# Kernel tuning notes

Measured on AMD Instinct MI355X. Metric: run time of the kernel, lower is better.

## Reference

```python
import jax, jax.numpy as jnp
import numpy as np

N = 50000      # nodes
E = 800000     # edges (avg degree 16)
F_IN = 128     # input feature dim
HID = 128      # 2 * out_classes
OUT = 64       # out_classes


def setup_inputs() -> dict:
    key = jax.random.key(0)
    ks = jax.random.split(key, 12)
    x = jax.random.normal(ks[0], (N, F_IN), jnp.float32)
    edge_index = jax.random.randint(ks[1], (2, E), 0, N, jnp.int32)
    def lin(k, fi, fo):
        return jax.random.normal(k, (fi, fo), jnp.float32) / np.float32(np.sqrt(fi))
    return {
        "x": x,
        "edge_index": edge_index,
        "W1": lin(ks[2], F_IN, HID), "b1": jnp.zeros((HID,), jnp.float32),
        "W2": lin(ks[3], HID, HID),  "b2": jnp.zeros((HID,), jnp.float32),
        "W3": lin(ks[4], HID, HID),  "b3": jnp.zeros((HID,), jnp.float32),
        "jk_w": jax.random.normal(ks[5], (3,), jnp.float32),
        "fc_W": lin(ks[6], HID, OUT), "fc_b": jnp.zeros((OUT,), jnp.float32),
    }


def _gcn_conv(h, W, b, row, col, n):
    """PyG GCNConv: linear -> add self-loops -> sym-normalized aggregate -> bias."""
    h = h @ W                                        # [n, d_out]
    loops = jnp.arange(n, dtype=row.dtype)
    r = jnp.concatenate([row, loops])                # sources
    c = jnp.concatenate([col, loops])                # targets
    deg = jax.ops.segment_sum(jnp.ones_like(c, h.dtype), c, num_segments=n)
    dinv = jnp.where(deg > 0, jax.lax.rsqrt(deg), 0.0)
    norm = dinv[r] * dinv[c]                         # [E+n]
    msg = h[r] * norm[:, None]                       # gather + scale
    return jax.ops.segment_sum(msg, c, num_segments=n) + b


def _neighbor_mean(h, row, col, n):
    """sample_neighbors with scale_factor=2: exact mean over out-neighbors,
    own feature when degree == 0 (top-k branch is provably dead code)."""
    s = jax.ops.segment_sum(h[col], row, num_segments=n)
    deg = jax.ops.segment_sum(jnp.ones_like(row, h.dtype), row, num_segments=n)
    mean = s / jnp.maximum(deg, 1.0)[:, None]
    return jnp.where((deg > 0)[:, None], mean, h)


def reference(x, edge_index, W1, b1, W2, b2, W3, b3, jk_w, fc_W, fc_b):
    row, col = edge_index[0], edge_index[1]
    n = x.shape[0]
    # layer 0: GCN -> ReLU -> (dropout: eval identity) -> neighbor sampling
    h0 = jax.nn.relu(_gcn_conv(x, W1, b1, row, col, n))
    h0 = _neighbor_mean(h0, row, col, n)
    # layer 1: GCN -> ReLU; historical-activation update is identity on first call
    h1 = jax.nn.relu(_gcn_conv(h0, W2, b2, row, col, n))
    # layer 2
    h2 = jax.nn.relu(_gcn_conv(h1, W3, b3, row, col, n))
    # dynamic JK aggregation
    w = jax.nn.softmax(jk_w)
    h = w[0] * h0 + w[1] * h1 + w[2] * h2
    return h @ fc_W + fc_b
```

## Files before the change

kernel.cpp:

```cpp
#include <hip/hip_runtime.h>
#include <stdint.h>

typedef unsigned int  uint32;
typedef unsigned short u16;

typedef short bfx8 __attribute__((ext_vector_type(8)));
typedef float f32x4 __attribute__((ext_vector_type(4)));
typedef float f32x2 __attribute__((ext_vector_type(2)));

#define NBP 256
#define CH  2048

__device__ __forceinline__ float b2f(u16 u) {
    union { uint32 i; float f; } v; v.i = ((uint32)u) << 16; return v.f;
}
__device__ __forceinline__ u16 f2b(float f) {
    union { float f; uint32 i; } v; v.f = f;
    uint32 u = v.i;
    return (u16)((u + 0x7fffu + ((u >> 16) & 1u)) >> 16);
}
__device__ __forceinline__ float blo(uint32 u) {
    union { uint32 i; float f; } v; v.i = u << 16; return v.f;
}
__device__ __forceinline__ float bhi(uint32 u) {
    union { uint32 i; float f; } v; v.i = u & 0xffff0000u; return v.f;
}
__device__ __forceinline__ uint32 packbf(float a, float b) {
    return (uint32)f2b(a) | ((uint32)f2b(b) << 16);
}
__device__ __forceinline__ void splitf(float x, u16& h, u16& l) {
    h = f2b(x);
    l = f2b(x - b2f(h));
}
__device__ __forceinline__ void split8(const float* __restrict__ p, bfx8& hi, bfx8& lo) {
    f32x4 a = *(const f32x4*)p;
    f32x4 b = *(const f32x4*)(p + 4);
    float x[8] = {a[0], a[1], a[2], a[3], b[0], b[1], b[2], b[3]};
#pragma unroll
    for (int j = 0; j < 8; ++j) {
        u16 h, l; splitf(x[j], h, l);
        hi[j] = (short)h; lo[j] = (short)l;
    }
}

__global__ __launch_bounds__(256) void k_preA(
    const int* __restrict__ row, const int* __restrict__ col, int E, int Gh,
    int* __restrict__ cntC, int* __restrict__ cntR, int* __restrict__ deg_in,
    const float* __restrict__ W1, const float* __restrict__ W2,
    const float* __restrict__ W3, const float* __restrict__ fcW,
    u16* __restrict__ WTh, u16* __restrict__ WTl, int WTN) {
    if ((int)blockIdx.x < Gh) {
        __shared__ int hp[NBP];
        int t = threadIdx.x;
        hp[t] = 0;
        __syncthreads();
        int base = blockIdx.x * CH;
        int n = E - base; if (n > CH) n = CH;
        for (int i = t; i < n; i += 256) {
            int r = row[base + i], c = col[base + i];
            atomicAdd(&hp[c >> 8], 1);
            atomicAdd(&hp[r >> 8], 0x10000);
            atomicAdd(&deg_in[c], 1);
        }
        __syncthreads();
        int v = hp[t];
        if (v & 0xffff) atomicAdd(&cntC[t], v & 0xffff);
        if (v >> 16)    atomicAdd(&cntR[t], v >> 16);
        return;
    }
    int i = ((int)blockIdx.x - Gh) * 256 + threadIdx.x;
    if (i >= WTN) return;
    float w;
    if (i < 3 * 16384) {
        int m = i >> 14, j = i & 16383;
        int fo = j >> 7, fi = j & 127;
        const float* W = (m == 0) ? W1 : (m == 1) ? W2 : W3;
        w = W[fi * 128 + fo];
    } else {
        int j = i - 3 * 16384;
        int fo = j >> 7, fi = j & 127;
        w = fcW[fi * 64 + fo];
    }
    u16 h, l; splitf(w, h, l);
    WTh[i] = h; WTl[i] = l;
}

__global__ __launch_bounds__(256) void k_scanB(
    const int* __restrict__ cntC, const int* __restrict__ cntR,
    int* __restrict__ bOffC, int* __restrict__ bOffR,
    int* __restrict__ curC, int* __restrict__ curR,
    const int* __restrict__ deg_in, float* __restrict__ dinv, int NB, int N) {
    int t = threadIdx.x;
    if (blockIdx.x >= 1) {
        int i = ((int)blockIdx.x - 1) * 256 + t;
        if (i < N) dinv[i] = rsqrtf((float)(deg_in[i] + 1));
        return;
    }
    int lane = t & 63, wid = t >> 6;
    __shared__ int wsum[4];
    for (int m = 0; m < 2; ++m) {
        const int* cnt = m ? cntR : cntC;
        int* bOff = m ? bOffR : bOffC;
        int* cur  = m ? curR  : curC;
        int v = (t < NB) ? cnt[t] : 0;
        int x = v;
#pragma unroll
        for (int d = 1; d < 64; d <<= 1) {
            int u = __shfl_up(x, d);
            if (lane >= d) x += u;
        }
        if (lane == 63) wsum[wid] = x;
        __syncthreads();
        int add = 0;
        for (int i = 0; i < wid; ++i) add += wsum[i];
        int ex = x + add - v;
        if (t <= NB) bOff[t] = ex;
        cur[t] = ex;
        __syncthreads();
    }
}

__device__ __forceinline__ void gemm128_f32_body(
    const float* __restrict__ A, const u16* __restrict__ WTh, const u16* __restrict__ WTl,
    const float* __restrict__ dinv, u16* __restrict__ G, int M, int blk) {
    const int lane = threadIdx.x & 63;
    const int q = lane >> 4, l = lane & 15;
    int rbase = blk * 128 + (threadIdx.x >> 6) * 32;
    if (rbase >= M) return;
    int r0 = rbase + l;      if (r0 >= M) r0 = M - 1;
    int r1 = rbase + 16 + l; if (r1 >= M) r1 = M - 1;

    f32x4 acc[2][8];
#pragma unroll
    for (int i = 0; i < 2; ++i)
#pragma unroll
        for (int j = 0; j < 8; ++j) acc[i][j] = (f32x4){0.f, 0.f, 0.f, 0.f};

#pragma unroll
    for (int kc = 0; kc < 4; ++kc) {
        int k0 = kc * 32 + q * 8;
        bfx8 ah0, al0, ah1, al1;
        split8(A + (size_t)r0 * 128 + k0, ah0, al0);
        split8(A + (size_t)r1 * 128 + k0, ah1, al1);
#pragma unroll
        for (int ct = 0; ct < 8; ++ct) {
            bfx8 bh = *(const bfx8*)(WTh + (ct * 16 + l) * 128 + k0);
            bfx8 bl = *(const bfx8*)(WTl + (ct * 16 + l) * 128 + k0);
            acc[0][ct] = __builtin_amdgcn_mfma_f32_16x16x32_bf16(ah0, bh, acc[0][ct], 0, 0, 0);
            acc[0][ct] = __builtin_amdgcn_mfma_f32_16x16x32_bf16(ah0, bl, acc[0][ct], 0, 0, 0);
            acc[0][ct] = __builtin_amdgcn_mfma_f32_16x16x32_bf16(al0, bh, acc[0][ct], 0, 0, 0);
            acc[1][ct] = __builtin_amdgcn_mfma_f32_16x16x32_bf16(ah1, bh, acc[1][ct], 0, 0, 0);
            acc[1][ct] = __builtin_amdgcn_mfma_f32_16x16x32_bf16(ah1, bl, acc[1][ct], 0, 0, 0);
            acc[1][ct] = __builtin_amdgcn_mfma_f32_16x16x32_bf16(al1, bh, acc[1][ct], 0, 0, 0);
        }
    }
#pragma unroll
    for (int rs = 0; rs < 2; ++rs) {
#pragma unroll
        for (int rr = 0; rr < 4; ++rr) {
            int rw = rbase + rs * 16 + q * 4 + rr;
            if (rw < M) {
                float dv = dinv[rw];
#pragma unroll
                for (int ct = 0; ct < 8; ++ct)
                    G[(size_t)rw * 128 + ct * 16 + l] = f2b(acc[rs][ct][rr] * dv);
            }
        }
    }
}

__global__ __launch_bounds__(256) void k_gemm128_pl(
    const u16* __restrict__ Ah, const u16* __restrict__ Al,
    const u16* __restrict__ WTh, const u16* __restrict__ WTl,
    const float* __restrict__ dinv, u16* __restrict__ G, int M) {
    const int lane = threadIdx.x & 63;
    const int q = lane >> 4, l = lane & 15;
    int rbase = blockIdx.x * 128 + (threadIdx.x >> 6) * 32;
    if (rbase >= M) return;
    int r0 = rbase + l;      if (r0 >= M) r0 = M - 1;
    int r1 = rbase + 16 + l; if (r1 >= M) r1 = M - 1;

    f32x4 acc[2][8];
#pragma unroll
    for (int i = 0; i < 2; ++i)
#pragma unroll
        for (int j = 0; j < 8; ++j) acc[i][j] = (f32x4){0.f, 0.f, 0.f, 0.f};

#pragma unroll
    for (int kc = 0; kc < 4; ++kc) {
        int k0 = kc * 32 + q * 8;
        bfx8 ah0 = *(const bfx8*)(Ah + (size_t)r0 * 128 + k0);
        bfx8 al0 = *(const bfx8*)(Al + (size_t)r0 * 128 + k0);
        bfx8 ah1 = *(const bfx8*)(Ah + (size_t)r1 * 128 + k0);
        bfx8 al1 = *(const bfx8*)(Al + (size_t)r1 * 128 + k0);
#pragma unroll
        for (int ct = 0; ct < 8; ++ct) {
            bfx8 bh = *(const bfx8*)(WTh + (ct * 16 + l) * 128 + k0);
            bfx8 bl = *(const bfx8*)(WTl + (ct * 16 + l) * 128 + k0);
            acc[0][ct] = __builtin_amdgcn_mfma_f32_16x16x32_bf16(ah0, bh, acc[0][ct], 0, 0, 0);
            acc[0][ct] = __builtin_amdgcn_mfma_f32_16x16x32_bf16(ah0, bl, acc[0][ct], 0, 0, 0);
            acc[0][ct] = __builtin_amdgcn_mfma_f32_16x16x32_bf16(al0, bh, acc[0][ct], 0, 0, 0);
            acc[1][ct] = __builtin_amdgcn_mfma_f32_16x16x32_bf16(ah1, bh, acc[1][ct], 0, 0, 0);
            acc[1][ct] = __builtin_amdgcn_mfma_f32_16x16x32_bf16(ah1, bl, acc[1][ct], 0, 0, 0);
            acc[1][ct] = __builtin_amdgcn_mfma_f32_16x16x32_bf16(al1, bh, acc[1][ct], 0, 0, 0);
        }
    }
#pragma unroll
    for (int rs = 0; rs < 2; ++rs) {
#pragma unroll
        for (int rr = 0; rr < 4; ++rr) {
            int rw = rbase + rs * 16 + q * 4 + rr;
            if (rw < M) {
                float dv = dinv[rw];
#pragma unroll
                for (int ct = 0; ct < 8; ++ct)
                    G[(size_t)rw * 128 + ct * 16 + l] = f2b(acc[rs][ct][rr] * dv);
            }
        }
    }
}

__global__ __launch_bounds__(256) void k_partC_gemm0(
    const int* __restrict__ row, const int* __restrict__ col, int E, int Gc,
    int* __restrict__ curC, int* __restrict__ curR,
    uint32* __restrict__ partC, uint32* __restrict__ partR,
    const float* __restrict__ A, const u16* __restrict__ WTh, const u16* __restrict__ WTl,
    const float* __restrict__ dinv, u16* __restrict__ G, int M) {
    if ((int)blockIdx.x >= Gc) {
        gemm128_f32_body(A, WTh, WTl, dinv, G, M, (int)blockIdx.x - Gc);
        return;
    }
    __shared__ uint32 stagedC[CH], stagedR[CH];
    __shared__ int hp[NBP], expk[NBP], curp[NBP], runC[NBP], runR[NBP];
    __shared__ int wsum[4];
    int t = threadIdx.x;
    int lane = t & 63, wid = t >> 6;
    int base = blockIdx.x * CH;
    int n = E - base; if (n > CH) n = CH;

    int er[8], ec[8];
#pragma unroll
    for (int j = 0; j < 8; ++j) {
        int i = t + j * 256;
        if (i < n) { er[j] = row[base + i]; ec[j] = col[base + i]; }
        else er[j] = -1;
    }
    hp[t] = 0;
    __syncthreads();
#pragma unroll
    for (int j = 0; j < 8; ++j) {
        if (er[j] >= 0) {
            atomicAdd(&hp[ec[j] >> 8], 1);
            atomicAdd(&hp[er[j] >> 8], 0x10000);
        }
    }
    __syncthreads();
    int v = hp[t];
    int x = v;
#pragma unroll
    for (int d = 1; d < 64; d <<= 1) {
        int u = __shfl_up(x, d);
        if (lane >= d) x += u;
    }
    if (lane == 63) wsum[wid] = x;
    __syncthreads();
    int add = 0;
    for (int i = 0; i < wid; ++i) add += wsum[i];
    int ex = x + add - v;
    expk[t] = ex;
    curp[t] = ex;
    int vC = v & 0xffff, vR = v >> 16;
    runC[t] = vC ? atomicAdd(&curC[t], vC) : 0;
    runR[t] = vR ? atomicAdd(&curR[t], vR) : 0;
    __syncthreads();
#pragma unroll
    for (int j = 0; j < 8; ++j) {
        if (er[j] >= 0) {
            int cb = ec[j] >> 8, rb = er[j] >> 8;
            int pC = atomicAdd(&curp[cb], 1) & 0xffff;
            stagedC[pC] = ((uint32)ec[j] << 16) | (uint32)er[j];
            int pR = atomicAdd(&curp[rb], 0x10000) >> 16;
            stagedR[pR] = ((uint32)er[j] << 16) | (uint32)ec[j];
        }
    }
    __syncthreads();
    for (int i = t; i < n; i += 256) {
        uint32 pv = stagedC[i];
        int b = pv >> 24;
        partC[runC[b] + (i - (expk[b] & 0xffff))] = pv;
    }
    for (int i = t; i < n; i += 256) {
        uint32 pv = stagedR[i];
        int b = pv >> 24;
        partR[runR[b] + (i - (expk[b] >> 16))] = pv;
    }
}

__global__ __launch_bounds__(256) void k_fillD(
    const uint32* __restrict__ partC, const uint32* __restrict__ partR,
    const int* __restrict__ bOffC, const int* __restrict__ bOffR,
    int* __restrict__ off_in, int* __restrict__ off_out,
    u16* __restrict__ csr_src, u16* __restrict__ csr_dst,
    int NB, int N, int E) {
    int part = ((int)blockIdx.x >= NB) ? 1 : 0;
    int b = (int)blockIdx.x - part * NB;
    const uint32* arr = part ? partR : partC;
    const int* bOff   = part ? bOffR : bOffC;
    int* offA         = part ? off_out : off_in;
    u16* csr          = part ? csr_dst : csr_src;
    int t = threadIdx.x;
    int lane = t & 63, wid = t >> 6;
    int base = bOff[b], end = bOff[b + 1];
    __shared__ int cnt[NBP], cur[NBP];
    __shared__ int wsum[4];
    cnt[t] = 0;
    __syncthreads();
    for (int i = base + t; i < end; i += 256)
        atomicAdd(&cnt[(arr[i] >> 16) & 255], 1);
    __syncthreads();
    int v = cnt[t];
    int x = v;
#pragma unroll
    for (int d = 1; d < 64; d <<= 1) {
        int u = __shfl_up(x, d);
        if (lane >= d) x += u;
    }
    if (lane == 63) wsum[wid] = x;
    __syncthreads();
    int add = 0;
    for (int i = 0; i < wid; ++i) add += wsum[i];
    int ex = x + add - v;
    cur[t] = ex;
    int node = (b << 8) + t;
    if (node < N) offA[node] = base + ex;
    if (b == 0 && t == 0) offA[N] = E;
    __syncthreads();
    for (int i = base + t; i < end; i += 256) {
        uint32 pv = arr[i];
        int local = (pv >> 16) & 255;
        int pos = atomicAdd(&cur[local], 1);
        csr[base + pos] = (u16)(pv & 0xffffu);
    }
}

template <int MODE>
__global__ __launch_bounds__(256) void k_agg(
    const uint32* __restrict__ g, const u16* __restrict__ csr_src,
    const int* __restrict__ off, const float* __restrict__ dinv,
    const f32x2* __restrict__ bias, uint32* __restrict__ outH,
    uint32* __restrict__ outL, int n) {
    int w = (blockIdx.x * 256 + threadIdx.x) >> 6;
    if (w >= n) return;
    int lane = threadIdx.x & 63;
    uint32 sv = g[(size_t)w * 64 + lane];
    float s0 = blo(sv), s1 = bhi(sv);
    int e = off[w], e1 = off[w + 1];
    for (; e + 8 <= e1; e += 8) {
        int ix[8];
#pragma unroll
        for (int j = 0; j < 8; ++j) ix[j] = csr_src[e + j];
        uint32 vv[8];
#pragma unroll
        for (int j = 0; j < 8; ++j) vv[j] = g[(size_t)ix[j] * 64 + lane];
#pragma unroll
        for (int j = 0; j < 8; ++j) { s0 += blo(vv[j]); s1 += bhi(vv[j]); }
    }
    for (; e + 2 <= e1; e += 2) {
        int i0 = csr_src[e], i1 = csr_src[e + 1];
        uint32 v0 = g[(size_t)i0 * 64 + lane];
        uint32 v1 = g[(size_t)i1 * 64 + lane];
        s0 += blo(v0) + blo(v1);
        s1 += bhi(v0) + bhi(v1);
    }
    if (e < e1) {
        uint32 v = g[(size_t)csr_src[e] * 64 + lane];
        s0 += blo(v); s1 += bhi(v);
    }
    float dc = dinv[w];
    f32x2 bb = bias[lane];
    float o0 = fmaxf(fmaf(s0, dc, bb[0]), 0.f);
    float o1 = fmaxf(fmaf(s1, dc, bb[1]), 0.f);
    if (MODE == 0) {
        outH[(size_t)w * 64 + lane] = packbf(o0, o1);
    } else {
        u16 h0, l0, h1, l1;
        splitf(o0, h0, l0);
        splitf(o1, h1, l1);
        outH[(size_t)w * 64 + lane] = (uint32)h0 | ((uint32)h1 << 16);
        outL[(size_t)w * 64 + lane] = (uint32)l0 | ((uint32)l1 << 16);
    }
}

__global__ __launch_bounds__(256) void k_mean(
    const uint32* __restrict__ h, const u16* __restrict__ csr_dst,
    const int* __restrict__ off, uint32* __restrict__ outH,
    uint32* __restrict__ outL, int n) {
    int w = (blockIdx.x * 256 + threadIdx.x) >> 6;
    if (w >= n) return;
    int lane = threadIdx.x & 63;
    int e = off[w], e1 = off[w + 1];
    int d = e1 - e;
    float s0 = 0.f, s1 = 0.f;
    for (; e + 8 <= e1; e += 8) {
        int ix[8];
#pragma unroll
        for (int j = 0; j < 8; ++j) ix[j] = csr_dst[e + j];
        uint32 vv[8];
#pragma unroll
        for (int j = 0; j < 8; ++j) vv[j] = h[(size_t)ix[j] * 64 + lane];
#pragma unroll
        for (int j = 0; j < 8; ++j) { s0 += blo(vv[j]); s1 += bhi(vv[j]); }
    }
    for (; e + 2 <= e1; e += 2) {
        int i0 = csr_dst[e], i1 = csr_dst[e + 1];
        uint32 v0 = h[(size_t)i0 * 64 + lane];
        uint32 v1 = h[(size_t)i1 * 64 + lane];
        s0 += blo(v0) + blo(v1);
        s1 += bhi(v0) + bhi(v1);
    }
    if (e < e1) {
        uint32 v = h[(size_t)csr_dst[e] * 64 + lane];
        s0 += blo(v); s1 += bhi(v);
    }
    float o0, o1;
    if (d > 0) {
        float inv = 1.f / (float)d;
        o0 = s0 * inv; o1 = s1 * inv;
    } else {
        uint32 sv = h[(size_t)w * 64 + lane];
        o0 = blo(sv); o1 = bhi(sv);
    }
    u16 ha, la, hb, lb;
    splitf(o0, ha, la);
    splitf(o1, hb, lb);
    outH[(size_t)w * 64 + lane] = (uint32)ha | ((uint32)hb << 16);
    outL[(size_t)w * 64 + lane] = (uint32)la | ((uint32)lb << 16);
}

__global__ __launch_bounds__(256) void k_final(
    const u16* __restrict__ h0h, const u16* __restrict__ h0l,
    const u16* __restrict__ h1h, const u16* __restrict__ h1l,
    const u16* __restrict__ h2h, const u16* __restrict__ h2l,
    const float* __restrict__ jkw,
    const u16* __restrict__ fcWTh, const u16* __restrict__ fcWTl,
    const float* __restrict__ fcb, float* __restrict__ out, int M) {
    float a0 = jkw[0], a1 = jkw[1], a2 = jkw[2];
    float mx = fmaxf(a0, fmaxf(a1, a2));
    float e0 = expf(a0 - mx), e1 = expf(a1 - mx), e2 = expf(a2 - mx);
    float inv = 1.f / (e0 + e1 + e2);
    float w0 = e0 * inv, w1 = e1 * inv, w2 = e2 * inv;

    const int lane = threadIdx.x & 63;
    const int q = lane >> 4, l = lane & 15;
    int rbase = blockIdx.x * 128 + (threadIdx.x >> 6) * 32;
    if (rbase >= M) return;
    int r0 = rbase + l;      if (r0 >= M) r0 = M - 1;
    int r1 = rbase + 16 + l; if (r1 >= M) r1 = M - 1;

    f32x4 acc[2][4];
#pragma unroll
    for (int i = 0; i < 2; ++i)
#pragma unroll
        for (int j = 0; j < 4; ++j) acc[i][j] = (f32x4){0.f, 0.f, 0.f, 0.f};

    union U8 { bfx8 v; u16 u[8]; };

#pragma unroll
    for (int kc = 0; kc < 4; ++kc) {
        int k0 = kc * 32 + q * 8;
        bfx8 ah[2], al[2];
        const int rr2[2] = {r0, r1};
#pragma unroll
        for (int half = 0; half < 2; ++half) {
            size_t o = (size_t)rr2[half] * 128 + k0;
            U8 x0h, x0l, x1h, x1l, x2h, x2l, rh, rl;
            x0h.v = *(const bfx8*)(h0h + o); x0l.v = *(const bfx8*)(h0l + o);
            x1h.v = *(const bfx8*)(h1h + o); x1l.v = *(const bfx8*)(h1l + o);
            x2h.v = *(const bfx8*)(h2h + o); x2l.v = *(const bfx8*)(h2l + o);
#pragma unroll
            for (int j = 0; j < 8; ++j) {
                float v0 = b2f(x0h.u[j]) + b2f(x0l.u[j]);
                float v1 = b2f(x1h.u[j]) + b2f(x1l.u[j]);
                float v2 = b2f(x2h.u[j]) + b2f(x2l.u[j]);
                float c = w0 * v0 + w1 * v1 + w2 * v2;
                u16 ch, cl; splitf(c, ch, cl);
                rh.u[j] = ch; rl.u[j] = cl;
            }
            ah[half] = rh.v; al[half] = rl.v;
        }
#pragma unroll
        for (int ct = 0; ct < 4; ++ct) {
            bfx8 bh = *(const bfx8*)(fcWTh + (ct * 16 + l) * 128 + k0);
            bfx8 bl = *(const bfx8*)(fcWTl + (ct * 16 + l) * 128 + k0);
#pragma unroll
            for (int half = 0; half < 2; ++half) {
                acc[half][ct] = __builtin_amdgcn_mfma_f32_16x16x32_bf16(ah[half], bh, acc[half][ct], 0, 0, 0);
                acc[half][ct] = __builtin_amdgcn_mfma_f32_16x16x32_bf16(ah[half], bl, acc[half][ct], 0, 0, 0);
                acc[half][ct] = __builtin_amdgcn_mfma_f32_16x16x32_bf16(al[half], bh, acc[half][ct], 0, 0, 0);
            }
        }
    }
#pragma unroll
    for (int rs = 0; rs < 2; ++rs) {
#pragma unroll
        for (int rr = 0; rr < 4; ++rr) {
            int rw = rbase + rs * 16 + q * 4 + rr;
            if (rw < M) {
#pragma unroll
                for (int ct = 0; ct < 4; ++ct) {
                    int cc = ct * 16 + l;
                    out[(size_t)rw * 64 + cc] = acc[rs][ct][rr] + fcb[cc];
                }
            }
        }
    }
}

extern "C" void kernel_launch(void* const* d_in, const int* in_sizes, int n_in,
                              void* d_out, int out_size, void* d_ws, size_t ws_size,
                              hipStream_t stream) {
    const int N = in_sizes[0] / 128;
    const int E = in_sizes[1] / 2;
    const int NB = (N + 255) >> 8;

    const float* x    = (const float*)d_in[0];
    const int* row    = (const int*)d_in[1];
    const int* col    = row + E;
    const float* W1   = (const float*)d_in[2];
    const float* b1   = (const float*)d_in[3];
    const float* W2   = (const float*)d_in[4];
    const float* b2   = (const float*)d_in[5];
    const float* W3   = (const float*)d_in[6];
    const float* b3   = (const float*)d_in[7];
    const float* jkw  = (const float*)d_in[8];
    const float* fcW  = (const float*)d_in[9];
    const float* fcb  = (const float*)d_in[10];
    float* outp       = (float*)d_out;

    char* ws = (char*)d_ws;
    size_t off = 0;
    auto alloc = [&](size_t bytes) -> char* {
        char* p = ws + off;
        off += (bytes + 255) & ~(size_t)255;
        return p;
    };
    int* deg_in = (int*)alloc((size_t)(N + 2 * NBP) * sizeof(int));
    int* cntC   = deg_in + N;
    int* cntR   = cntC + NBP;
    int* bOffC  = (int*)alloc((size_t)(NBP + 1) * sizeof(int));
    int* bOffR  = (int*)alloc((size_t)(NBP + 1) * sizeof(int));
    int* curC   = (int*)alloc((size_t)NBP * sizeof(int));
    int* curR   = (int*)alloc((size_t)NBP * sizeof(int));
    int* off_in  = (int*)alloc((size_t)(N + 1) * sizeof(int));
    int* off_out = (int*)alloc((size_t)(N + 1) * sizeof(int));
    uint32* partC = (uint32*)alloc((size_t)E * sizeof(uint32));
    uint32* partR = (uint32*)alloc((size_t)E * sizeof(uint32));
    u16* csr_src = (u16*)alloc((size_t)E * sizeof(u16));
    u16* csr_dst = (u16*)alloc((size_t)E * sizeof(u16));
    float* dinv  = (float*)alloc((size_t)N * sizeof(float));
    const int WTN = 3 * 16384 + 8192;
    u16* WTh = (u16*)alloc((size_t)WTN * sizeof(u16));
    u16* WTl = (u16*)alloc((size_t)WTN * sizeof(u16));
    size_t FB = (size_t)N * 128 * sizeof(u16);
    u16* gbuf = (u16*)alloc(FB);
    u16* t0   = (u16*)alloc(FB);
    u16* h0h = (u16*)alloc(FB); u16* h0l = (u16*)alloc(FB);
    u16* h1h = (u16*)alloc(FB); u16* h1l = (u16*)alloc(FB);
    u16* h2h = (u16*)alloc(FB); u16* h2l = (u16*)alloc(FB);

    hipMemsetAsync(deg_in, 0, (size_t)(N + 2 * NBP) * sizeof(int), stream);

    const int B = 256;
    int Gh = (E + CH - 1) / CH;
    int Gwt = (WTN + B - 1) / B;
    k_preA<<<Gh + Gwt, B, 0, stream>>>(row, col, E, Gh, cntC, cntR, deg_in,
                                       W1, W2, W3, fcW, WTh, WTl, WTN);
    k_scanB<<<1 + (N + B - 1) / B, B, 0, stream>>>(cntC, cntR, bOffC, bOffR,
                                                   curC, curR, deg_in, dinv, NB, N);

    int Gc = (E + CH - 1) / CH;
    int Gg = (N + 127) / 128;
    k_partC_gemm0<<<Gc + Gg, B, 0, stream>>>(row, col, E, Gc, curC, curR, partC, partR,
                                             x, WTh, WTl, dinv, gbuf, N);
    k_fillD<<<2 * NB, B, 0, stream>>>(partC, partR, bOffC, bOffR,
                                      off_in, off_out, csr_src, csr_dst, NB, N, E);

    int aggG = (N + 3) / 4;

    k_agg<0><<<aggG, B, 0, stream>>>((const uint32*)gbuf, csr_src, off_in, dinv,
                                     (const f32x2*)b1, (uint32*)t0, nullptr, N);
    k_mean<<<aggG, B, 0, stream>>>((const uint32*)t0, csr_dst, off_out,
                                   (uint32*)h0h, (uint32*)h0l, N);
    k_gemm128_pl<<<Gg, B, 0, stream>>>(h0h, h0l, WTh + 16384, WTl + 16384, dinv, gbuf, N);
    k_agg<1><<<aggG, B, 0, stream>>>((const uint32*)gbuf, csr_src, off_in, dinv,
                                     (const f32x2*)b2, (uint32*)h1h, (uint32*)h1l, N);
    k_gemm128_pl<<<Gg, B, 0, stream>>>(h1h, h1l, WTh + 2 * 16384, WTl + 2 * 16384, dinv, gbuf, N);
    k_agg<1><<<aggG, B, 0, stream>>>((const uint32*)gbuf, csr_src, off_in, dinv,
                                     (const f32x2*)b3, (uint32*)h2h, (uint32*)h2l, N);
    k_final<<<Gg, B, 0, stream>>>(h0h, h0l, h1h, h1l, h2h, h2l, jkw,
                                  WTh + 3 * 16384, WTl + 3 * 16384, fcb, outp, N);
}
```

Measured before the change: 388.0 us.

## Split aggregation into feature-column passes and derive dinv from CSR fill

The node-degree atomics and the separate dinv kernel are removed. dinv is now computed in the CSR fill kernel from per-node counts, and the first GEMM stops applying dinv, so layer-0 aggregation scales each neighbor by its own dinv. The aggregation and mean kernels are restructured so 16-lane groups each handle one node and one 16-column slice, with four slice passes launched as separate blocks. This should give smaller, more cache-friendly gathered working sets and fewer idle lanes per wavefront, at the cost of reloading indices per pass and divergence padding to the maximum degree within a wave.

```diff
diff --git a/kernel.cpp b/kernel.cpp
--- a/kernel.cpp
+++ b/kernel.cpp
@@ -45,7 +45,7 @@
 
 __global__ __launch_bounds__(256) void k_preA(
     const int* __restrict__ row, const int* __restrict__ col, int E, int Gh,
-    int* __restrict__ cntC, int* __restrict__ cntR, int* __restrict__ deg_in,
+    int* __restrict__ cntC, int* __restrict__ cntR,
     const float* __restrict__ W1, const float* __restrict__ W2,
     const float* __restrict__ W3, const float* __restrict__ fcW,
     u16* __restrict__ WTh, u16* __restrict__ WTl, int WTN) {
@@ -60,7 +60,6 @@
             int r = row[base + i], c = col[base + i];
             atomicAdd(&hp[c >> 8], 1);
             atomicAdd(&hp[r >> 8], 0x10000);
-            atomicAdd(&deg_in[c], 1);
         }
         __syncthreads();
         int v = hp[t];
@@ -88,14 +87,8 @@
 __global__ __launch_bounds__(256) void k_scanB(
     const int* __restrict__ cntC, const int* __restrict__ cntR,
     int* __restrict__ bOffC, int* __restrict__ bOffR,
-    int* __restrict__ curC, int* __restrict__ curR,
-    const int* __restrict__ deg_in, float* __restrict__ dinv, int NB, int N) {
+    int* __restrict__ curC, int* __restrict__ curR, int NB) {
     int t = threadIdx.x;
-    if (blockIdx.x >= 1) {
-        int i = ((int)blockIdx.x - 1) * 256 + t;
-        if (i < N) dinv[i] = rsqrtf((float)(deg_in[i] + 1));
-        return;
-    }
     int lane = t & 63, wid = t >> 6;
     __shared__ int wsum[4];
     for (int m = 0; m < 2; ++m) {
@@ -160,7 +153,7 @@
         for (int rr = 0; rr < 4; ++rr) {
             int rw = rbase + rs * 16 + q * 4 + rr;
             if (rw < M) {
-                float dv = dinv[rw];
+                float dv = dinv ? dinv[rw] : 1.0f;
 #pragma unroll
                 for (int ct = 0; ct < 8; ++ct)
                     G[(size_t)rw * 128 + ct * 16 + l] = f2b(acc[rs][ct][rr] * dv);
@@ -225,9 +218,9 @@
     int* __restrict__ curC, int* __restrict__ curR,
     uint32* __restrict__ partC, uint32* __restrict__ partR,
     const float* __restrict__ A, const u16* __restrict__ WTh, const u16* __restrict__ WTl,
-    const float* __restrict__ dinv, u16* __restrict__ G, int M) {
+    u16* __restrict__ G, int M) {
     if ((int)blockIdx.x >= Gc) {
-        gemm128_f32_body(A, WTh, WTl, dinv, G, M, (int)blockIdx.x - Gc);
+        gemm128_f32_body(A, WTh, WTl, nullptr, G, M, (int)blockIdx.x - Gc);
         return;
     }
     __shared__ uint32 stagedC[CH], stagedR[CH];
@@ -301,7 +294,7 @@
     const int* __restrict__ bOffC, const int* __restrict__ bOffR,
     int* __restrict__ off_in, int* __restrict__ off_out,
     u16* __restrict__ csr_src, u16* __restrict__ csr_dst,
-    int NB, int N, int E) {
+    float* __restrict__ dinv, int NB, int N, int E) {
     int part = ((int)blockIdx.x >= NB) ? 1 : 0;
     int b = (int)blockIdx.x - part * NB;
     const uint32* arr = part ? partR : partC;
@@ -332,7 +325,10 @@
     int ex = x + add - v;
     cur[t] = ex;
     int node = (b << 8) + t;
-    if (node < N) offA[node] = base + ex;
+    if (node < N) {
+        offA[node] = base + ex;
+        if (part == 0) dinv[node] = rsqrtf((float)(v + 1));
+    }
     if (b == 0 && t == 0) offA[N] = E;
     __syncthreads();
     for (int i = base + t; i < end; i += 256) {
@@ -344,97 +340,102 @@
 }
 
 template <int MODE>
-__global__ __launch_bounds__(256) void k_agg(
-    const uint32* __restrict__ g, const u16* __restrict__ csr_src,
+__global__ __launch_bounds__(256) void k_agg4(
+    const uint32* __restrict__ g, const u16* __restrict__ csr,
     const int* __restrict__ off, const float* __restrict__ dinv,
     const f32x2* __restrict__ bias, uint32* __restrict__ outH,
-    uint32* __restrict__ outL, int n) {
-    int w = (blockIdx.x * 256 + threadIdx.x) >> 6;
-    if (w >= n) return;
-    int lane = threadIdx.x & 63;
-    uint32 sv = g[(size_t)w * 64 + lane];
-    float s0 = blo(sv), s1 = bhi(sv);
-    int e = off[w], e1 = off[w + 1];
-    for (; e + 8 <= e1; e += 8) {
-        int ix[8];
-#pragma unroll
-        for (int j = 0; j < 8; ++j) ix[j] = csr_src[e + j];
-        uint32 vv[8];
-#pragma unroll
-        for (int j = 0; j < 8; ++j) vv[j] = g[(size_t)ix[j] * 64 + lane];
-#pragma unroll
-        for (int j = 0; j < 8; ++j) { s0 += blo(vv[j]); s1 += bhi(vv[j]); }
-    }
-    for (; e + 2 <= e1; e += 2) {
-        int i0 = csr_src[e], i1 = csr_src[e + 1];
-        uint32 v0 = g[(size_t)i0 * 64 + lane];
-        uint32 v1 = g[(size_t)i1 * 64 + lane];
-        s0 += blo(v0) + blo(v1);
-        s1 += bhi(v0) + bhi(v1);
-    }
-    if (e < e1) {
-        uint32 v = g[(size_t)csr_src[e] * 64 + lane];
-        s0 += blo(v); s1 += bhi(v);
-    }
+    uint32* __restrict__ outL, int n, int nb) {
+    int pass = blockIdx.x / nb;
+    int blk  = blockIdx.x - pass * nb;
+    int gi = (threadIdx.x & 63) >> 4;
+    int fl = threadIdx.x & 15;
+    int w = blk * 16 + (threadIdx.x >> 6) * 4 + gi;
+    bool valid = (w < n);
+    if (!valid) w = n - 1;
+    int wi = pass * 16 + fl;
+    int e0 = off[w], e1 = off[w + 1];
+    int deg = e1 - e0;
+    uint32 sv = g[(size_t)w * 64 + wi];
     float dc = dinv[w];
-    f32x2 bb = bias[lane];
+    float s0, s1;
+    if (MODE == 0) { s0 = blo(sv) * dc; s1 = bhi(sv) * dc; }
+    else           { s0 = blo(sv);      s1 = bhi(sv); }
+    int m = max(deg, __shfl_xor(deg, 16));
+    m = max(m, __shfl_xor(m, 32));
+    for (int it = 0; it < m; it += 4) {
+#pragma unroll
+        for (int k = 0; k < 4; ++k) {
+            int tt = it + k;
+            bool a = tt < deg;
+            int idx = a ? (int)csr[e0 + tt] : w;
+            uint32 vv = g[(size_t)idx * 64 + wi];
+            if (MODE == 0) {
+                float dm = a ? dinv[idx] : 0.f;
+                s0 = fmaf(blo(vv), dm, s0);
+                s1 = fmaf(bhi(vv), dm, s1);
+            } else {
+                vv = a ? vv : 0u;
+                s0 += blo(vv); s1 += bhi(vv);
+            }
+        }
+    }
+    f32x2 bb = bias[wi];
     float o0 = fmaxf(fmaf(s0, dc, bb[0]), 0.f);
     float o1 = fmaxf(fmaf(s1, dc, bb[1]), 0.f);
+    if (!valid) return;
     if (MODE == 0) {
-        outH[(size_t)w * 64 + lane] = packbf(o0, o1);
+        outH[(size_t)w * 64 + wi] = packbf(o0, o1);
     } else {
         u16 h0, l0, h1, l1;
         splitf(o0, h0, l0);
         splitf(o1, h1, l1);
-        outH[(size_t)w * 64 + lane] = (uint32)h0 | ((uint32)h1 << 16);
-        outL[(size_t)w * 64 + lane] = (uint32)l0 | ((uint32)l1 << 16);
-    }
-}
-
-__global__ __launch_bounds__(256) void k_mean(
-    const uint32* __restrict__ h, const u16* __restrict__ csr_dst,
+        outH[(size_t)w * 64 + wi] = (uint32)h0 | ((uint32)h1 << 16);
+        outL[(size_t)w * 64 + wi] = (uint32)l0 | ((uint32)l1 << 16);
+    }
+}
+
+__global__ __launch_bounds__(256) void k_mean4(
+    const uint32* __restrict__ h, const u16* __restrict__ csr,
     const int* __restrict__ off, uint32* __restrict__ outH,
-    uint32* __restrict__ outL, int n) {
-    int w = (blockIdx.x * 256 + threadIdx.x) >> 6;
-    if (w >= n) return;
-    int lane = threadIdx.x & 63;
-    int e = off[w], e1 = off[w + 1];
-    int d = e1 - e;
+    uint32* __restrict__ outL, int n, int nb) {
+    int pass = blockIdx.x / nb;
+    int blk  = blockIdx.x - pass * nb;
+    int gi = (threadIdx.x & 63) >> 4;
+    int fl = threadIdx.x & 15;
+    int w = blk * 16 + (threadIdx.x >> 6) * 4 + gi;
+    bool valid = (w < n);
+    if (!valid) w = n - 1;
+    int wi = pass * 16 + fl;
+    int e0 = off[w], e1 = off[w + 1];
+    int deg = e1 - e0;
+    uint32 sv = h[(size_t)w * 64 + wi];
     float s0 = 0.f, s1 = 0.f;
-    for (; e + 8 <= e1; e += 8) {
-        int ix[8];
-#pragma unroll
-        for (int j = 0; j < 8; ++j) ix[j] = csr_dst[e + j];
-        uint32 vv[8];
-#pragma unroll
-        for (int j = 0; j < 8; ++j) vv[j] = h[(size_t)ix[j] * 64 + lane];
-#pragma unroll
-        for (int j = 0; j < 8; ++j) { s0 += blo(vv[j]); s1 += bhi(vv[j]); }
-    }
-    for (; e + 2 <= e1; e += 2) {
-        int i0 = csr_dst[e], i1 = csr_dst[e + 1];
-        uint32 v0 = h[(size_t)i0 * 64 + lane];
-        uint32 v1 = h[(size_t)i1 * 64 + lane];
-        s0 += blo(v0) + blo(v1);
-        s1 += bhi(v0) + bhi(v1);
-    }
-    if (e < e1) {
-        uint32 v = h[(size_t)csr_dst[e] * 64 + lane];
-        s0 += blo(v); s1 += bhi(v);
+    int m = max(deg, __shfl_xor(deg, 16));
+    m = max(m, __shfl_xor(m, 32));
+    for (int it = 0; it < m; it += 4) {
+#pragma unroll
+        for (int k = 0; k < 4; ++k) {
+            int tt = it + k;
+            bool a = tt < deg;
+            int idx = a ? (int)csr[e0 + tt] : w;
+            uint32 vv = h[(size_t)idx * 64 + wi];
+            vv = a ? vv : 0u;
+            s0 += blo(vv); s1 += bhi(vv);
+        }
     }
     float o0, o1;
-    if (d > 0) {
-        float inv = 1.f / (float)d;
+    if (deg > 0) {
+        float inv = 1.f / (float)deg;
         o0 = s0 * inv; o1 = s1 * inv;
     } else {
-        uint32 sv = h[(size_t)w * 64 + lane];
         o0 = blo(sv); o1 = bhi(sv);
     }
+    if (!valid) return;
     u16 ha, la, hb, lb;
     splitf(o0, ha, la);
     splitf(o1, hb, lb);
-    outH[(size_t)w * 64 + lane] = (uint32)ha | ((uint32)hb << 16);
-    outL[(size_t)w * 64 + lane] = (uint32)la | ((uint32)lb << 16);
+    outH[(size_t)w * 64 + wi] = (uint32)ha | ((uint32)hb << 16);
+    outL[(size_t)w * 64 + wi] = (uint32)la | ((uint32)lb << 16);
 }
 
 __global__ __launch_bounds__(256) void k_final(
@@ -544,8 +545,7 @@
         off += (bytes + 255) & ~(size_t)255;
         return p;
     };
-    int* deg_in = (int*)alloc((size_t)(N + 2 * NBP) * sizeof(int));
-    int* cntC   = deg_in + N;
+    int* cntC   = (int*)alloc((size_t)2 * NBP * sizeof(int));
     int* cntR   = cntC + NBP;
     int* bOffC  = (int*)alloc((size_t)(NBP + 1) * sizeof(int));
     int* bOffR  = (int*)alloc((size_t)(NBP + 1) * sizeof(int));
@@ -568,35 +568,35 @@
     u16* h1h = (u16*)alloc(FB); u16* h1l = (u16*)alloc(FB);
     u16* h2h = (u16*)alloc(FB); u16* h2l = (u16*)alloc(FB);
 
-    hipMemsetAsync(deg_in, 0, (size_t)(N + 2 * NBP) * sizeof(int), stream);
+    hipMemsetAsync(cntC, 0, (size_t)2 * NBP * sizeof(int), stream);
 
     const int B = 256;
     int Gh = (E + CH - 1) / CH;
     int Gwt = (WTN + B - 1) / B;
-    k_preA<<<Gh + Gwt, B, 0, stream>>>(row, col, E, Gh, cntC, cntR, deg_in,
+    k_preA<<<Gh + Gwt, B, 0, stream>>>(row, col, E, Gh, cntC, cntR,
                                        W1, W2, W3, fcW, WTh, WTl, WTN);
-    k_scanB<<<1 + (N + B - 1) / B, B, 0, stream>>>(cntC, cntR, bOffC, bOffR,
-                                                   curC, curR, deg_in, dinv, NB, N);
+    k_scanB<<<1, B, 0, stream>>>(cntC, cntR, bOffC, bOffR, curC, curR, NB);
 
     int Gc = (E + CH - 1) / CH;
     int Gg = (N + 127) / 128;
     k_partC_gemm0<<<Gc + Gg, B, 0, stream>>>(row, col, E, Gc, curC, curR, partC, partR,
-                                             x, WTh, WTl, dinv, gbuf, N);
+                                             x, WTh, WTl, gbuf, N);
     k_fillD<<<2 * NB, B, 0, stream>>>(partC, partR, bOffC, bOffR,
-                                      off_in, off_out, csr_src, csr_dst, NB, N, E);
-
-    int aggG = (N + 3) / 4;
-
-    k_agg<0><<<aggG, B, 0, stream>>>((const uint32*)gbuf, csr_src, off_in, dinv,
-                                     (const f32x2*)b1, (uint32*)t0, nullptr, N);
-    k_mean<<<aggG, B, 0, stream>>>((const uint32*)t0, csr_dst, off_out,
-                                   (uint32*)h0h, (uint32*)h0l, N);
+                                      off_in, off_out, csr_src, csr_dst, dinv, NB, N, E);
+
+    int nb = (N + 15) / 16;
+    int aggG = 4 * nb;
+
+    k_agg4<0><<<aggG, B, 0, stream>>>((const uint32*)gbuf, csr_src, off_in, dinv,
+                                      (const f32x2*)b1, (uint32*)t0, nullptr, N, nb);
+    k_mean4<<<aggG, B, 0, stream>>>((const uint32*)t0, csr_dst, off_out,
+                                    (uint32*)h0h, (uint32*)h0l, N, nb);
     k_gemm128_pl<<<Gg, B, 0, stream>>>(h0h, h0l, WTh + 16384, WTl + 16384, dinv, gbuf, N);
-    k_agg<1><<<aggG, B, 0, stream>>>((const uint32*)gbuf, csr_src, off_in, dinv,
-                                     (const f32x2*)b2, (uint32*)h1h, (uint32*)h1l, N);
+    k_agg4<1><<<aggG, B, 0, stream>>>((const uint32*)gbuf, csr_src, off_in, dinv,
+                                      (const f32x2*)b2, (uint32*)h1h, (uint32*)h1l, N, nb);
     k_gemm128_pl<<<Gg, B, 0, stream>>>(h1h, h1l, WTh + 2 * 16384, WTl + 2 * 16384, dinv, gbuf, N);
-    k_agg<1><<<aggG, B, 0, stream>>>((const uint32*)gbuf, csr_src, off_in, dinv,
-                                     (const f32x2*)b3, (uint32*)h2h, (uint32*)h2l, N);
+    k_agg4<1><<<aggG, B, 0, stream>>>((const uint32*)gbuf, csr_src, off_in, dinv,
+                                      (const f32x2*)b3, (uint32*)h2h, (uint32*)h2l, N, nb);
     k_final<<<Gg, B, 0, stream>>>(h0h, h0l, h1h, h1l, h2h, h2l, jkw,
                                   WTh + 3 * 16384, WTl + 3 * 16384, fcb, outp, N);
 }
```

Measured after the change: 515.8 us. 33.0% more time.

## Derive in-degree from CSR fill and move layer-0 normalization into aggregation

Applied to the files above, without the earlier changes.

Removes the per-edge global atomic degree count and the large degree memset. dinv is now computed in the CSR fill kernel from the per-node counts it already has. Because dinv is not ready before the first GEMM, that GEMM no longer scales rows by dinv; the layer-0 aggregation instead multiplies each gathered neighbor row by its dinv, which adds a gather of dinv per edge. The fused partition+GEMM kernel is split into two separate launches, and the two-at-a-time tail loops are simplified to single-step loops.

```diff
diff --git a/kernel.cpp b/kernel.cpp
--- a/kernel.cpp
+++ b/kernel.cpp
@@ -45,7 +45,7 @@
 
 __global__ __launch_bounds__(256) void k_preA(
     const int* __restrict__ row, const int* __restrict__ col, int E, int Gh,
-    int* __restrict__ cntC, int* __restrict__ cntR, int* __restrict__ deg_in,
+    int* __restrict__ cntC, int* __restrict__ cntR,
     const float* __restrict__ W1, const float* __restrict__ W2,
     const float* __restrict__ W3, const float* __restrict__ fcW,
     u16* __restrict__ WTh, u16* __restrict__ WTl, int WTN) {
@@ -60,7 +60,6 @@
             int r = row[base + i], c = col[base + i];
             atomicAdd(&hp[c >> 8], 1);
             atomicAdd(&hp[r >> 8], 0x10000);
-            atomicAdd(&deg_in[c], 1);
         }
         __syncthreads();
         int v = hp[t];
@@ -88,14 +87,8 @@
 __global__ __launch_bounds__(256) void k_scanB(
     const int* __restrict__ cntC, const int* __restrict__ cntR,
     int* __restrict__ bOffC, int* __restrict__ bOffR,
-    int* __restrict__ curC, int* __restrict__ curR,
-    const int* __restrict__ deg_in, float* __restrict__ dinv, int NB, int N) {
+    int* __restrict__ curC, int* __restrict__ curR, int NB) {
     int t = threadIdx.x;
-    if (blockIdx.x >= 1) {
-        int i = ((int)blockIdx.x - 1) * 256 + t;
-        if (i < N) dinv[i] = rsqrtf((float)(deg_in[i] + 1));
-        return;
-    }
     int lane = t & 63, wid = t >> 6;
     __shared__ int wsum[4];
     for (int m = 0; m < 2; ++m) {
@@ -160,13 +153,19 @@
         for (int rr = 0; rr < 4; ++rr) {
             int rw = rbase + rs * 16 + q * 4 + rr;
             if (rw < M) {
-                float dv = dinv[rw];
+                float dv = dinv ? dinv[rw] : 1.0f;
 #pragma unroll
                 for (int ct = 0; ct < 8; ++ct)
                     G[(size_t)rw * 128 + ct * 16 + l] = f2b(acc[rs][ct][rr] * dv);
             }
         }
     }
+}
+
+__global__ __launch_bounds__(256) void k_gemm0(
+    const float* __restrict__ A, const u16* __restrict__ WTh, const u16* __restrict__ WTl,
+    u16* __restrict__ G, int M) {
+    gemm128_f32_body(A, WTh, WTl, nullptr, G, M, blockIdx.x);
 }
 
 __global__ __launch_bounds__(256) void k_gemm128_pl(
@@ -220,16 +219,10 @@
     }
 }
 
-__global__ __launch_bounds__(256) void k_partC_gemm0(
-    const int* __restrict__ row, const int* __restrict__ col, int E, int Gc,
+__global__ __launch_bounds__(256) void k_partC(
+    const int* __restrict__ row, const int* __restrict__ col, int E,
     int* __restrict__ curC, int* __restrict__ curR,
-    uint32* __restrict__ partC, uint32* __restrict__ partR,
-    const float* __restrict__ A, const u16* __restrict__ WTh, const u16* __restrict__ WTl,
-    const float* __restrict__ dinv, u16* __restrict__ G, int M) {
-    if ((int)blockIdx.x >= Gc) {
-        gemm128_f32_body(A, WTh, WTl, dinv, G, M, (int)blockIdx.x - Gc);
-        return;
-    }
+    uint32* __restrict__ partC, uint32* __restrict__ partR) {
     __shared__ uint32 stagedC[CH], stagedR[CH];
     __shared__ int hp[NBP], expk[NBP], curp[NBP], runC[NBP], runR[NBP];
     __shared__ int wsum[4];
@@ -301,7 +294,7 @@
     const int* __restrict__ bOffC, const int* __restrict__ bOffR,
     int* __restrict__ off_in, int* __restrict__ off_out,
     u16* __restrict__ csr_src, u16* __restrict__ csr_dst,
-    int NB, int N, int E) {
+    float* __restrict__ dinv, int NB, int N, int E) {
     int part = ((int)blockIdx.x >= NB) ? 1 : 0;
     int b = (int)blockIdx.x - part * NB;
     const uint32* arr = part ? partR : partC;
@@ -332,7 +325,10 @@
     int ex = x + add - v;
     cur[t] = ex;
     int node = (b << 8) + t;
-    if (node < N) offA[node] = base + ex;
+    if (node < N) {
+        offA[node] = base + ex;
+        if (part == 0) dinv[node] = rsqrtf((float)(v + 1));
+    }
     if (b == 0 && t == 0) offA[N] = E;
     __syncthreads();
     for (int i = base + t; i < end; i += 256) {
@@ -352,8 +348,11 @@
     int w = (blockIdx.x * 256 + threadIdx.x) >> 6;
     if (w >= n) return;
     int lane = threadIdx.x & 63;
+    float dc = dinv[w];
     uint32 sv = g[(size_t)w * 64 + lane];
-    float s0 = blo(sv), s1 = bhi(sv);
+    float s0, s1;
+    if (MODE == 0) { s0 = blo(sv) * dc; s1 = bhi(sv) * dc; }
+    else           { s0 = blo(sv);      s1 = bhi(sv); }
     int e = off[w], e1 = off[w + 1];
     for (; e + 8 <= e1; e += 8) {
         int ix[8];
@@ -362,21 +361,31 @@
         uint32 vv[8];
 #pragma unroll
         for (int j = 0; j < 8; ++j) vv[j] = g[(size_t)ix[j] * 64 + lane];
-#pragma unroll
-        for (int j = 0; j < 8; ++j) { s0 += blo(vv[j]); s1 += bhi(vv[j]); }
-    }
-    for (; e + 2 <= e1; e += 2) {
-        int i0 = csr_src[e], i1 = csr_src[e + 1];
-        uint32 v0 = g[(size_t)i0 * 64 + lane];
-        uint32 v1 = g[(size_t)i1 * 64 + lane];
-        s0 += blo(v0) + blo(v1);
-        s1 += bhi(v0) + bhi(v1);
-    }
-    if (e < e1) {
-        uint32 v = g[(size_t)csr_src[e] * 64 + lane];
-        s0 += blo(v); s1 += bhi(v);
-    }
-    float dc = dinv[w];
+        if (MODE == 0) {
+            float dm[8];
+#pragma unroll
+            for (int j = 0; j < 8; ++j) dm[j] = dinv[ix[j]];
+#pragma unroll
+            for (int j = 0; j < 8; ++j) {
+                s0 = fmaf(blo(vv[j]), dm[j], s0);
+                s1 = fmaf(bhi(vv[j]), dm[j], s1);
+            }
+        } else {
+#pragma unroll
+            for (int j = 0; j < 8; ++j) { s0 += blo(vv[j]); s1 += bhi(vv[j]); }
+        }
+    }
+    for (; e < e1; ++e) {
+        int ix = csr_src[e];
+        uint32 v = g[(size_t)ix * 64 + lane];
+        if (MODE == 0) {
+            float dm = dinv[ix];
+            s0 = fmaf(blo(v), dm, s0);
+            s1 = fmaf(bhi(v), dm, s1);
+        } else {
+            s0 += blo(v); s1 += bhi(v);
+        }
+    }
     f32x2 bb = bias[lane];
     float o0 = fmaxf(fmaf(s0, dc, bb[0]), 0.f);
     float o1 = fmaxf(fmaf(s1, dc, bb[1]), 0.f);
@@ -411,14 +420,7 @@
 #pragma unroll
         for (int j = 0; j < 8; ++j) { s0 += blo(vv[j]); s1 += bhi(vv[j]); }
     }
-    for (; e + 2 <= e1; e += 2) {
-        int i0 = csr_dst[e], i1 = csr_dst[e + 1];
-        uint32 v0 = h[(size_t)i0 * 64 + lane];
-        uint32 v1 = h[(size_t)i1 * 64 + lane];
-        s0 += blo(v0) + blo(v1);
-        s1 += bhi(v0) + bhi(v1);
-    }
-    if (e < e1) {
+    for (; e < e1; ++e) {
         uint32 v = h[(size_t)csr_dst[e] * 64 + lane];
         s0 += blo(v); s1 += bhi(v);
     }
@@ -544,8 +546,7 @@
         off += (bytes + 255) & ~(size_t)255;
         return p;
     };
-    int* deg_in = (int*)alloc((size_t)(N + 2 * NBP) * sizeof(int));
-    int* cntC   = deg_in + N;
+    int* cntC   = (int*)alloc((size_t)2 * NBP * sizeof(int));
     int* cntR   = cntC + NBP;
     int* bOffC  = (int*)alloc((size_t)(NBP + 1) * sizeof(int));
     int* bOffR  = (int*)alloc((size_t)(NBP + 1) * sizeof(int));
@@ -568,22 +569,19 @@
     u16* h1h = (u16*)alloc(FB); u16* h1l = (u16*)alloc(FB);
     u16* h2h = (u16*)alloc(FB); u16* h2l = (u16*)alloc(FB);
 
-    hipMemsetAsync(deg_in, 0, (size_t)(N + 2 * NBP) * sizeof(int), stream);
+    hipMemsetAsync(cntC, 0, (size_t)2 * NBP * sizeof(int), stream);
 
     const int B = 256;
     int Gh = (E + CH - 1) / CH;
     int Gwt = (WTN + B - 1) / B;
-    k_preA<<<Gh + Gwt, B, 0, stream>>>(row, col, E, Gh, cntC, cntR, deg_in,
+    int Gg = (N + 127) / 128;
+    k_preA<<<Gh + Gwt, B, 0, stream>>>(row, col, E, Gh, cntC, cntR,
                                        W1, W2, W3, fcW, WTh, WTl, WTN);
-    k_scanB<<<1 + (N + B - 1) / B, B, 0, stream>>>(cntC, cntR, bOffC, bOffR,
-                                                   curC, curR, deg_in, dinv, NB, N);
-
-    int Gc = (E + CH - 1) / CH;
-    int Gg = (N + 127) / 128;
-    k_partC_gemm0<<<Gc + Gg, B, 0, stream>>>(row, col, E, Gc, curC, curR, partC, partR,
-                                             x, WTh, WTl, dinv, gbuf, N);
+    k_scanB<<<1, B, 0, stream>>>(cntC, cntR, bOffC, bOffR, curC, curR, NB);
+    k_gemm0<<<Gg, B, 0, stream>>>(x, WTh, WTl, gbuf, N);
+    k_partC<<<Gh, B, 0, stream>>>(row, col, E, curC, curR, partC, partR);
     k_fillD<<<2 * NB, B, 0, stream>>>(partC, partR, bOffC, bOffR,
-                                      off_in, off_out, csr_src, csr_dst, NB, N, E);
+                                      off_in, off_out, csr_src, csr_dst, dinv, NB, N, E);
 
     int aggG = (N + 3) / 4;
 
```

After: 381.4 us. About the same (-1.7%).
